# Optimization experiments

Measured on AMD Instinct MI355X. Metric: run time of the kernel, lower is better.

## Reference

```python
import jax, jax.numpy as jnp
import numpy as np

FORGET_BIAS = 1.0
LAYERS = 2


def setup_inputs() -> dict:
    key = jax.random.key(0)
    ks = jax.random.split(key, 10)
    B, T, H, V = 64, 50, 256, 50000
    G = 4 * H
    s = 1.0 / np.sqrt(H)
    return {
        "input_data": jax.random.randint(ks[0], (B, T), 0, V, dtype=jnp.int64),
        "embedding": jax.random.uniform(ks[1], (V, H), jnp.float32, -1.0, 1.0),
        "Wx": jax.random.normal(ks[2], (LAYERS, H, G), jnp.float32) * s,
        "Uh": jax.random.normal(ks[3], (LAYERS, H, G), jnp.float32) * s,
        "alpha": jax.random.uniform(ks[4], (LAYERS, G), jnp.float32),
        "beta1": jax.random.uniform(ks[5], (LAYERS, G), jnp.float32),
        "beta2": jax.random.uniform(ks[6], (LAYERS, G), jnp.float32),
        "bias": jnp.zeros((LAYERS, G), jnp.float32),
        "softmax_w": jax.random.normal(ks[7], (V, H), jnp.float32) * s,
        "softmax_b": jnp.full((V,), 0.1, jnp.float32),
    }


def _mi_lstm_stack(inputs_tbh, Wx, Uh, alpha, beta1, beta2, bias):
    # inputs_tbh: [T, B, H]; params have leading layer axis [L, ...]
    T, B, H = inputs_tbh.shape
    c0 = jnp.zeros((LAYERS, B, H), inputs_tbh.dtype)
    h0 = jnp.zeros((LAYERS, B, H), inputs_tbh.dtype)

    def step(carry, x_t):
        c, h = carry
        inp = x_t
        new_c, new_h = [], []
        for l in range(LAYERS):
            xh = inp @ Wx[l]          # [B, 4H]
            hh = h[l] @ Uh[l]         # [B, 4H]
            gates = alpha[l] * xh * hh + beta1[l] * xh + beta2[l] * hh + bias[l]
            i, j, f, o = jnp.split(gates, 4, axis=-1)
            c_l = c[l] * jax.nn.sigmoid(f + FORGET_BIAS) + jax.nn.sigmoid(i) * jnp.tanh(j)
            h_l = jnp.tanh(c_l) * jax.nn.sigmoid(o)
            new_c.append(c_l)
            new_h.append(h_l)
            inp = h_l
        return (jnp.stack(new_c), jnp.stack(new_h)), inp

    (_, _), outs = jax.lax.scan(step, (c0, h0), inputs_tbh)
    return outs  # [T, B, H] top-layer hidden states


def reference(input_data, embedding, Wx, Uh, alpha, beta1, beta2, bias, softmax_w, softmax_b):
    # embedding lookup: [B, T, H] -> time-major [T, B, H]
    x = embedding[input_data]
    outs = _mi_lstm_stack(jnp.transpose(x, (1, 0, 2)), Wx, Uh, alpha, beta1, beta2, bias)
    # batch-major flatten like tf.reshape(outputs, [-1, rnn_size]) on [B, T, H]
    H = outs.shape[-1]
    flat = jnp.transpose(outs, (1, 0, 2)).reshape(-1, H)  # [B*T, H]
    logits = flat @ softmax_w.T + softmax_b               # [B*T, V]
    return logits
```

## Files before the change

### kernel.cpp

```cpp
#include <hip/hip_runtime.h>
#include <hip/hip_bf16.h>
#include <math.h>

#define B_ 64
#define T_ 50
#define H_ 256
#define G_ 1024
#define V_ 50000
#define NBLK 32

using f16x8 = __attribute__((ext_vector_type(8))) _Float16;
using f32x4 = __attribute__((ext_vector_type(4))) float;

__device__ __forceinline__ float sigm(float x) { return 1.0f / (1.0f + expf(-x)); }

__global__ __launch_bounds__(64) void embed_k(const int* __restrict__ idx,
                                              const float* __restrict__ emb,
                                              float* __restrict__ x_tm)
{
    const int row = blockIdx.x;
    const int b = row & (B_ - 1);
    const int t = row >> 6;
    const int id = idx[b * T_ + t];
    const float4 v = *reinterpret_cast<const float4*>(emb + (size_t)id * H_ + threadIdx.x * 4);
    *reinterpret_cast<float4*>(x_tm + (size_t)row * H_ + threadIdx.x * 4) = v;
}

__global__ __launch_bounds__(256) void conv_half(const float* __restrict__ in,
                                                 _Float16* __restrict__ out, int n)
{
    const int i = (blockIdx.x * 256 + threadIdx.x) * 8;
    if (i + 8 <= n) {
        const float4 v0 = *reinterpret_cast<const float4*>(in + i);
        const float4 v1 = *reinterpret_cast<const float4*>(in + i + 4);
        f16x8 h;
        h[0] = (_Float16)v0.x; h[1] = (_Float16)v0.y;
        h[2] = (_Float16)v0.z; h[3] = (_Float16)v0.w;
        h[4] = (_Float16)v1.x; h[5] = (_Float16)v1.y;
        h[6] = (_Float16)v1.z; h[7] = (_Float16)v1.w;
        *reinterpret_cast<f16x8*>(out + i) = h;
    }
}

__global__ __launch_bounds__(256) void pack_w_rec(const float* __restrict__ Uh0,
                                                  const float* __restrict__ Wx1,
                                                  const float* __restrict__ Uh1,
                                                  _Float16* __restrict__ wpk)
{
    const int c = blockIdx.x;
    const int m = blockIdx.y;
    const float* __restrict__ src = (m == 0) ? Uh0 : (m == 1) ? Wx1 : Uh1;
    _Float16* __restrict__ dst = wpk + (((size_t)c * 3 + m) << 13);
    for (int i = threadIdx.x; i < 8192; i += 256) {
        const int k = i >> 5;
        const int col = i & 31;
        const int colg = ((col >> 3) << 8) + (c << 3) + (col & 7);
        dst[(col << 8) + k] = (_Float16)src[(size_t)k * G_ + colg];
    }
}

__global__ __launch_bounds__(256) void gemm128_kn(const float* __restrict__ A,
                                                  const float* __restrict__ Bm,
                                                  float* __restrict__ C,
                                                  int M, int N, int K)
{
    __shared__ float As[32][132];
    __shared__ float Bs[32][132];

    const int m0 = blockIdx.x * 128;
    const int n0 = blockIdx.y * 128;
    const int tid = threadIdx.x;
    const int tm = (tid >> 4) << 3;
    const int tn = (tid & 15) << 3;

    float acc[8][8];
#pragma unroll
    for (int i = 0; i < 8; ++i)
#pragma unroll
        for (int j = 0; j < 8; ++j) acc[i][j] = 0.0f;

    for (int k0 = 0; k0 < K; k0 += 32) {
#pragma unroll
        for (int i = 0; i < 4; ++i) {
            const int s = tid + (i << 8);
            const int m = s >> 3;
            const int kk = (s & 7) << 2;
            const float4 v = *reinterpret_cast<const float4*>(
                A + (size_t)(m0 + m) * K + k0 + kk);
            As[kk + 0][m] = v.x; As[kk + 1][m] = v.y;
            As[kk + 2][m] = v.z; As[kk + 3][m] = v.w;
        }
#pragma unroll
        for (int i = 0; i < 4; ++i) {
            const int s = tid + (i << 8);
            const int kk = s >> 5;
            const int nn = (s & 31) << 2;
            const float4 v = *reinterpret_cast<const float4*>(
                Bm + (size_t)(k0 + kk) * N + n0 + nn);
            *reinterpret_cast<float4*>(&Bs[kk][nn]) = v;
        }
        __syncthreads();

#pragma unroll
        for (int k = 0; k < 32; ++k) {
            float a[8], bb[8];
            *reinterpret_cast<float4*>(&a[0]) = *reinterpret_cast<const float4*>(&As[k][tm]);
            *reinterpret_cast<float4*>(&a[4]) = *reinterpret_cast<const float4*>(&As[k][tm + 4]);
            *reinterpret_cast<float4*>(&bb[0]) = *reinterpret_cast<const float4*>(&Bs[k][tn]);
            *reinterpret_cast<float4*>(&bb[4]) = *reinterpret_cast<const float4*>(&Bs[k][tn + 4]);
#pragma unroll
            for (int i = 0; i < 8; ++i)
#pragma unroll
                for (int j = 0; j < 8; ++j)
                    acc[i][j] = fmaf(a[i], bb[j], acc[i][j]);
        }
        __syncthreads();
    }

#pragma unroll
    for (int i = 0; i < 8; ++i) {
        const int m = m0 + tm + i;
#pragma unroll
        for (int j = 0; j < 8; j += 4) {
            const int n = n0 + tn + j;
            float4 v;
            v.x = acc[i][j + 0]; v.y = acc[i][j + 1];
            v.z = acc[i][j + 2]; v.w = acc[i][j + 3];
            *reinterpret_cast<float4*>(C + (size_t)m * N + n) = v;
        }
    }
}

__device__ __forceinline__ void gbar_arrive(int* slot)
{
    __syncthreads();
    if (threadIdx.x == 0) {
        __threadfence();
        __hip_atomic_fetch_add(slot, 1, __ATOMIC_RELAXED, __HIP_MEMORY_SCOPE_AGENT);
    }
}

__device__ __forceinline__ void gbar_wait(int* slot)
{
    if (threadIdx.x == 0) {
        while (__hip_atomic_load(slot, __ATOMIC_RELAXED, __HIP_MEMORY_SCOPE_AGENT) < NBLK)
            __builtin_amdgcn_s_sleep(1);
    }
    __syncthreads();
    __threadfence();
}

__global__ __launch_bounds__(256) void mi_rec(
    const _Float16* __restrict__ wpk,
    const float* __restrict__ xh0,
    _Float16* __restrict__ h0x,
    _Float16* __restrict__ h1x,
    _Float16* __restrict__ outsH,
    int* __restrict__ bars,
    const float* __restrict__ alpha, const float* __restrict__ b1,
    const float* __restrict__ b2, const float* __restrict__ bsv)
{
    __shared__ __align__(16) _Float16 h0l[16384];
    __shared__ __align__(16) _Float16 h1l[16384];
    __shared__ __align__(16) _Float16 wl[24576];
    __shared__ float gA[2112], gB[2112];
    __shared__ float c0l[512], c1l[512];

    const int c = blockIdx.x;
    const int tid = threadIdx.x;
    const int l = tid & 63;
    const int w = tid >> 6;

    for (int i = tid; i < 2048; i += 256) {
        *reinterpret_cast<f16x8*>(&h0l[i << 3]) = f16x8{};
        *reinterpret_cast<f16x8*>(&h1l[i << 3]) = f16x8{};
    }
    for (int i = tid; i < 512; i += 256) { c0l[i] = 0.f; c1l[i] = 0.f; }

    for (int i = tid; i < 3072; i += 256) {
        const int m = i >> 10;
        const int col = (i >> 5) & 31;
        const int ch = i & 31;
        const f16x8 v = *reinterpret_cast<const f16x8*>(
            &wpk[(((size_t)c * 3 + m) * 32 + col) * 256 + (ch << 3)]);
        *reinterpret_cast<f16x8*>(
            &wl[(m * 32 + col) * 256 + ((ch ^ (col & 7)) << 3)]) = v;
    }

    const int u = tid & 7, b0 = tid >> 3;
    const int jl = (c << 3) + u;
    float al0[4], b10[4], b20[4], bs0[4], al1[4], b11[4], b21[4], bs1[4];
#pragma unroll
    for (int g = 0; g < 4; ++g) {
        const int col = (g << 8) + jl;
        al0[g] = alpha[col];        b10[g] = b1[col];
        b20[g] = b2[col];           bs0[g] = bsv[col];
        al1[g] = alpha[G_ + col];   b11[g] = b1[G_ + col];
        b21[g] = b2[G_ + col];      bs1[g] = bsv[G_ + col];
    }
    __syncthreads();

    const int arow = (w << 4) + (l & 15);
    const int cA = l & 15, cB = 16 + (l & 15);
    const int kq = l >> 4;

    auto MM = [&](const _Float16* __restrict__ am, const _Float16* __restrict__ bm,
                  f32x4& A0, f32x4& A1) {
#pragma unroll
        for (int s = 0; s < 8; ++s) {
            const int ck = (s << 2) + kq;
            const f16x8 af = *reinterpret_cast<const f16x8*>(
                &am[(arow << 8) + ((ck ^ (arow & 7)) << 3)]);
            const f16x8 bf0 = *reinterpret_cast<const f16x8*>(
                &bm[(cA << 8) + ((ck ^ (cA & 7)) << 3)]);
            const f16x8 bf1 = *reinterpret_cast<const f16x8*>(
                &bm[(cB << 8) + ((ck ^ (cB & 7)) << 3)]);
            A0 = __builtin_amdgcn_mfma_f32_16x16x32_f16(af, bf0, A0, 0, 0, 0);
            A1 = __builtin_amdgcn_mfma_f32_16x16x32_f16(af, bf1, A1, 0, 0, 0);
        }
    };

    auto STG = [&](float* gl, f32x4 A0, f32x4 A1) {
        const int rb = (w << 4) + (kq << 2);
#pragma unroll
        for (int r = 0; r < 4; ++r) {
            gl[(rb + r) * 33 + cA] = A0[r];
            gl[(rb + r) * 33 + cB] = A1[r];
        }
    };

    auto STAGE_H = [&](const _Float16* __restrict__ src, _Float16* __restrict__ dst) {
#pragma unroll
        for (int it = 0; it < 8; ++it) {
            const int idx = (it << 8) + tid;
            const int row = idx >> 5, ch = idx & 31;
            const f16x8 v = *reinterpret_cast<const f16x8*>(&src[(row << 8) + (ch << 3)]);
            *reinterpret_cast<f16x8*>(&dst[(row << 8) + ((ch ^ (row & 7)) << 3)]) = v;
        }
    };

    for (int s = 0; s <= T_; ++s) {
        const int p = s & 1;
        _Float16* __restrict__ h0w = h0x + (p << 14);
        _Float16* __restrict__ h1w = h1x + (p << 14);

        if (s < T_) {
            f32x4 A0 = {}, A1 = {};
            MM(h0l, wl, A0, A1);
            STG(gA, A0, A1);
            __syncthreads();
#pragma unroll
            for (int bb = 0; bb < 2; ++bb) {
                const int b = b0 + (bb << 5);
                float g4[4];
#pragma unroll
                for (int g = 0; g < 4; ++g) {
                    const float a = gA[b * 33 + (g << 3) + u];
                    const float x = xh0[(((size_t)(s * B_ + b)) << 10) + (g << 8) + jl];
                    g4[g] = al0[g] * x * a + b10[g] * x + b20[g] * a + bs0[g];
                }
                const float cn = c0l[(b << 3) + u] * sigm(g4[2] + 1.f)
                               + sigm(g4[0]) * tanhf(g4[1]);
                c0l[(b << 3) + u] = cn;
                h0w[(b << 8) + jl] = (_Float16)(tanhf(cn) * sigm(g4[3]));
            }
            __syncthreads();
        }

        if (s > 0) {
            f32x4 X0 = {}, X1 = {}, H0 = {}, H1 = {};
            MM(h0l, wl + 1 * 8192, X0, X1);
            MM(h1l, wl + 2 * 8192, H0, H1);
            STG(gA, X0, X1);
            STG(gB, H0, H1);
            __syncthreads();
#pragma unroll
            for (int bb = 0; bb < 2; ++bb) {
                const int b = b0 + (bb << 5);
                float g4[4];
#pragma unroll
                for (int g = 0; g < 4; ++g) {
                    const float xa = gA[b * 33 + (g << 3) + u];
                    const float ha = gB[b * 33 + (g << 3) + u];
                    g4[g] = al1[g] * xa * ha + b11[g] * xa + b21[g] * ha + bs1[g];
                }
                const float cn = c1l[(b << 3) + u] * sigm(g4[2] + 1.f)
                               + sigm(g4[0]) * tanhf(g4[1]);
                c1l[(b << 3) + u] = cn;
                const float hn = tanhf(cn) * sigm(g4[3]);
                h1w[(b << 8) + jl] = (_Float16)hn;
                outsH[(((size_t)b * T_ + (s - 1)) << 8) + jl] = (_Float16)hn;
            }
        }

        if (s < T_) {
            gbar_arrive(&bars[s]);
            gbar_wait(&bars[s]);
            STAGE_H(h0w, h0l);
            if (s > 0) STAGE_H(h1w, h1l);
            __syncthreads();
        }
    }
}

#define PM 128
#define PN 128
#define PK 64

__device__ __forceinline__ void gload_lds16(const void* g, void* l)
{
    __builtin_amdgcn_global_load_lds(
        (const __attribute__((address_space(1))) unsigned int*)g,
        (__attribute__((address_space(3))) unsigned int*)l, 16, 0, 0);
}

__global__ __launch_bounds__(256) void proj_mfma(
    const _Float16* __restrict__ A16,
    const _Float16* __restrict__ B16,
    const float* __restrict__ bias,
    float* __restrict__ C)
{
    __shared__ __align__(16) _Float16 Asub[PM * PK];
    __shared__ __align__(16) _Float16 Bsub[PN * PK];

    const int tid = threadIdx.x;
    const int l = tid & 63;
    const int w = tid >> 6;
    const int wm = w >> 1, wn = w & 1;

    const int n0 = blockIdx.x * PN;
    const int m0 = blockIdx.y * PM;

    f32x4 acc[4][4] = {};

    for (int k0 = 0; k0 < H_; k0 += PK) {
#pragma unroll
        for (int is = 0; is < 4; ++is) {
            const int i = is * 256 + tid;
            const int r = i >> 3;
            const int ch = (i & 7) ^ (r & 7);
            gload_lds16(A16 + (size_t)(m0 + r) * H_ + k0 + ch * 8, &Asub[i * 8]);
            int n = n0 + r; if (n > V_ - 1) n = V_ - 1;
            gload_lds16(B16 + (size_t)n * H_ + k0 + ch * 8, &Bsub[i * 8]);
        }
        __syncthreads();

#pragma unroll
        for (int ks = 0; ks < 2; ++ks) {
            f16x8 af[4], bf[4];
#pragma unroll
            for (int i = 0; i < 4; ++i) {
                const int r = wm * 64 + i * 16 + (l & 15);
                const int ch = (ks * 4 + (l >> 4)) ^ (r & 7);
                af[i] = *reinterpret_cast<const f16x8*>(&Asub[r * PK + ch * 8]);
            }
#pragma unroll
            for (int jf = 0; jf < 4; ++jf) {
                const int r = wn * 64 + jf * 16 + (l & 15);
                const int ch = (ks * 4 + (l >> 4)) ^ (r & 7);
                bf[jf] = *reinterpret_cast<const f16x8*>(&Bsub[r * PK + ch * 8]);
            }
#pragma unroll
            for (int i = 0; i < 4; ++i)
#pragma unroll
                for (int jf = 0; jf < 4; ++jf)
                    acc[i][jf] = __builtin_amdgcn_mfma_f32_16x16x32_f16(
                        af[i], bf[jf], acc[i][jf], 0, 0, 0);
        }
        __syncthreads();
    }

    const int rb = (l >> 4) << 2;
    const int cl = l & 15;
#pragma unroll
    for (int jf = 0; jf < 4; ++jf) {
        const int col = n0 + wn * 64 + jf * 16 + cl;
        if (col < V_) {
            const float bv = bias[col];
#pragma unroll
            for (int i = 0; i < 4; ++i) {
                const int rowb = m0 + wm * 64 + i * 16 + rb;
#pragma unroll
                for (int r = 0; r < 4; ++r)
                    C[(size_t)(rowb + r) * V_ + col] = acc[i][jf][r] + bv;
            }
        }
    }
}

extern "C" void kernel_launch(void* const* d_in, const int* in_sizes, int n_in,
                              void* d_out, int out_size, void* d_ws, size_t ws_size,
                              hipStream_t stream)
{
    const int*   idx   = (const int*)  d_in[0];
    const float* emb   = (const float*)d_in[1];
    const float* Wx    = (const float*)d_in[2];
    const float* Uh    = (const float*)d_in[3];
    const float* alpha = (const float*)d_in[4];
    const float* b1    = (const float*)d_in[5];
    const float* b2    = (const float*)d_in[6];
    const float* bsv   = (const float*)d_in[7];
    const float* sw    = (const float*)d_in[8];
    const float* sb    = (const float*)d_in[9];
    float* out = (float*)d_out;

    char* wsb = (char*)d_ws;
    float*    x_tm  = (float*)   (wsb);
    float*    xh0   = (float*)   (wsb + 3276800);
    _Float16* outsH = (_Float16*)(wsb + 16384000);
    _Float16* w16   = (_Float16*)(wsb + 18022400);
    _Float16* wpk   = (_Float16*)(wsb + 43622400);
    _Float16* h0x   = (_Float16*)(wsb + 45195264);
    _Float16* h1x   = (_Float16*)(wsb + 45260800);
    int*      bars  = (int*)     (wsb + 45326336);

    const float* Wx1 = Wx + (size_t)H_ * G_;
    const float* Uh0 = Uh;
    const float* Uh1 = Uh + (size_t)H_ * G_;

    hipMemsetAsync(bars, 0, 512, stream);

    {
        dim3 grid(NBLK, 3);
        pack_w_rec<<<grid, 256, 0, stream>>>(Uh0, Wx1, Uh1, wpk);
    }

    conv_half<<<(V_ * H_) / 2048, 256, 0, stream>>>(sw, w16, V_ * H_);

    embed_k<<<T_ * B_, 64, 0, stream>>>(idx, emb, x_tm);

    {
        dim3 grid(3200 / 128, G_ / 128);
        gemm128_kn<<<grid, 256, 0, stream>>>(x_tm, Wx, xh0, 3200, G_, H_);
    }

    mi_rec<<<NBLK, 256, 0, stream>>>(wpk, xh0, h0x, h1x, outsH, bars,
                                     alpha, b1, b2, bsv);

    {
        dim3 grid((V_ + PN - 1) / PN, 3200 / PM);
        proj_mfma<<<grid, 256, 0, stream>>>(outsH, w16, sb, out);
    }
}
```

Baseline: 724.1 us.

## Use fp16 MFMA for input GEMM, pad barrier slots, reorder projection grid

```diff
diff --git a/kernel.cpp b/kernel.cpp
--- a/kernel.cpp
+++ b/kernel.cpp
@@ -8,22 +8,27 @@
 #define G_ 1024
 #define V_ 50000
 #define NBLK 32
+#define BSTRIDE 64
 
 using f16x8 = __attribute__((ext_vector_type(8))) _Float16;
+using f16x4 = __attribute__((ext_vector_type(4))) _Float16;
 using f32x4 = __attribute__((ext_vector_type(4))) float;
 
 __device__ __forceinline__ float sigm(float x) { return 1.0f / (1.0f + expf(-x)); }
 
 __global__ __launch_bounds__(64) void embed_k(const int* __restrict__ idx,
                                               const float* __restrict__ emb,
-                                              float* __restrict__ x_tm)
+                                              _Float16* __restrict__ x16)
 {
     const int row = blockIdx.x;
     const int b = row & (B_ - 1);
     const int t = row >> 6;
     const int id = idx[b * T_ + t];
     const float4 v = *reinterpret_cast<const float4*>(emb + (size_t)id * H_ + threadIdx.x * 4);
-    *reinterpret_cast<float4*>(x_tm + (size_t)row * H_ + threadIdx.x * 4) = v;
+    f16x4 h;
+    h[0] = (_Float16)v.x; h[1] = (_Float16)v.y;
+    h[2] = (_Float16)v.z; h[3] = (_Float16)v.w;
+    *reinterpret_cast<f16x4*>(x16 + (size_t)row * H_ + threadIdx.x * 4) = h;
 }
 
 __global__ __launch_bounds__(256) void conv_half(const float* __restrict__ in,
@@ -42,6 +47,27 @@
     }
 }
 
+__global__ __launch_bounds__(256) void pack_wx0(const float* __restrict__ Wx0,
+                                                _Float16* __restrict__ wxT)
+{
+    __shared__ _Float16 ts[64][65];
+    const int k0 = blockIdx.x * 64;
+    const int n0 = blockIdx.y * 64;
+    const int tr = threadIdx.x >> 6;
+    const int tc = threadIdx.x & 63;
+#pragma unroll
+    for (int i = 0; i < 16; ++i) {
+        const int r = i * 4 + tr;
+        ts[r][tc] = (_Float16)Wx0[(size_t)(k0 + r) * G_ + n0 + tc];
+    }
+    __syncthreads();
+#pragma unroll
+    for (int i = 0; i < 16; ++i) {
+        const int c = i * 4 + tr;
+        wxT[(size_t)(n0 + c) * H_ + k0 + tc] = ts[tc][c];
+    }
+}
+
 __global__ __launch_bounds__(256) void pack_w_rec(const float* __restrict__ Uh0,
                                                   const float* __restrict__ Wx1,
                                                   const float* __restrict__ Uh1,
@@ -59,76 +85,11 @@
     }
 }
 
-__global__ __launch_bounds__(256) void gemm128_kn(const float* __restrict__ A,
-                                                  const float* __restrict__ Bm,
-                                                  float* __restrict__ C,
-                                                  int M, int N, int K)
-{
-    __shared__ float As[32][132];
-    __shared__ float Bs[32][132];
-
-    const int m0 = blockIdx.x * 128;
-    const int n0 = blockIdx.y * 128;
-    const int tid = threadIdx.x;
-    const int tm = (tid >> 4) << 3;
-    const int tn = (tid & 15) << 3;
-
-    float acc[8][8];
-#pragma unroll
-    for (int i = 0; i < 8; ++i)
-#pragma unroll
-        for (int j = 0; j < 8; ++j) acc[i][j] = 0.0f;
-
-    for (int k0 = 0; k0 < K; k0 += 32) {
-#pragma unroll
-        for (int i = 0; i < 4; ++i) {
-            const int s = tid + (i << 8);
-            const int m = s >> 3;
-            const int kk = (s & 7) << 2;
-            const float4 v = *reinterpret_cast<const float4*>(
-                A + (size_t)(m0 + m) * K + k0 + kk);
-            As[kk + 0][m] = v.x; As[kk + 1][m] = v.y;
-            As[kk + 2][m] = v.z; As[kk + 3][m] = v.w;
-        }
-#pragma unroll
-        for (int i = 0; i < 4; ++i) {
-            const int s = tid + (i << 8);
-            const int kk = s >> 5;
-            const int nn = (s & 31) << 2;
-            const float4 v = *reinterpret_cast<const float4*>(
-                Bm + (size_t)(k0 + kk) * N + n0 + nn);
-            *reinterpret_cast<float4*>(&Bs[kk][nn]) = v;
-        }
-        __syncthreads();
-
-#pragma unroll
-        for (int k = 0; k < 32; ++k) {
-            float a[8], bb[8];
-            *reinterpret_cast<float4*>(&a[0]) = *reinterpret_cast<const float4*>(&As[k][tm]);
-            *reinterpret_cast<float4*>(&a[4]) = *reinterpret_cast<const float4*>(&As[k][tm + 4]);
-            *reinterpret_cast<float4*>(&bb[0]) = *reinterpret_cast<const float4*>(&Bs[k][tn]);
-            *reinterpret_cast<float4*>(&bb[4]) = *reinterpret_cast<const float4*>(&Bs[k][tn + 4]);
-#pragma unroll
-            for (int i = 0; i < 8; ++i)
-#pragma unroll
-                for (int j = 0; j < 8; ++j)
-                    acc[i][j] = fmaf(a[i], bb[j], acc[i][j]);
-        }
-        __syncthreads();
-    }
-
-#pragma unroll
-    for (int i = 0; i < 8; ++i) {
-        const int m = m0 + tm + i;
-#pragma unroll
-        for (int j = 0; j < 8; j += 4) {
-            const int n = n0 + tn + j;
-            float4 v;
-            v.x = acc[i][j + 0]; v.y = acc[i][j + 1];
-            v.z = acc[i][j + 2]; v.w = acc[i][j + 3];
-            *reinterpret_cast<float4*>(C + (size_t)m * N + n) = v;
-        }
-    }
+__device__ __forceinline__ void gload_lds16(const void* g, void* l)
+{
+    __builtin_amdgcn_global_load_lds(
+        (const __attribute__((address_space(1))) unsigned int*)g,
+        (__attribute__((address_space(3))) unsigned int*)l, 16, 0, 0);
 }
 
 __device__ __forceinline__ void gbar_arrive(int* slot)
@@ -140,7 +101,7 @@
     }
 }
 
-__device__ __forceinline__ void gbar_wait(int* slot)
+__device__ __forceinline__ void gbar_wait_fast(int* slot)
 {
     if (threadIdx.x == 0) {
         while (__hip_atomic_load(slot, __ATOMIC_RELAXED, __HIP_MEMORY_SCOPE_AGENT) < NBLK)
@@ -148,6 +109,79 @@
     }
     __syncthreads();
     __threadfence();
+}
+
+#define PM 128
+#define PN 128
+#define PK 64
+
+__global__ __launch_bounds__(256) void gemm16_mfma(
+    const _Float16* __restrict__ A16,
+    const _Float16* __restrict__ B16,
+    float* __restrict__ C)
+{
+    __shared__ __align__(16) _Float16 Asub[PM * PK];
+    __shared__ __align__(16) _Float16 Bsub[PN * PK];
+
+    const int tid = threadIdx.x;
+    const int l = tid & 63;
+    const int w = tid >> 6;
+    const int wm = w >> 1, wn = w & 1;
+
+    const int n0 = blockIdx.x * PN;
+    const int m0 = blockIdx.y * PM;
+
+    f32x4 acc[4][4] = {};
+
+    for (int k0 = 0; k0 < H_; k0 += PK) {
+#pragma unroll
+        for (int is = 0; is < 4; ++is) {
+            const int i = is * 256 + tid;
+            const int r = i >> 3;
+            const int ch = (i & 7) ^ (r & 7);
+            gload_lds16(A16 + (size_t)(m0 + r) * H_ + k0 + ch * 8, &Asub[i * 8]);
+            gload_lds16(B16 + (size_t)(n0 + r) * H_ + k0 + ch * 8, &Bsub[i * 8]);
+        }
+        __syncthreads();
+
+#pragma unroll
+        for (int ks = 0; ks < 2; ++ks) {
+            f16x8 af[4], bf[4];
+#pragma unroll
+            for (int i = 0; i < 4; ++i) {
+                const int r = wm * 64 + i * 16 + (l & 15);
+                const int ch = (ks * 4 + (l >> 4)) ^ (r & 7);
+                af[i] = *reinterpret_cast<const f16x8*>(&Asub[r * PK + ch * 8]);
+            }
+#pragma unroll
+            for (int jf = 0; jf < 4; ++jf) {
+                const int r = wn * 64 + jf * 16 + (l & 15);
+                const int ch = (ks * 4 + (l >> 4)) ^ (r & 7);
+                bf[jf] = *reinterpret_cast<const f16x8*>(&Bsub[r * PK + ch * 8]);
+            }
+#pragma unroll
+            for (int i = 0; i < 4; ++i)
+#pragma unroll
+                for (int jf = 0; jf < 4; ++jf)
+                    acc[i][jf] = __builtin_amdgcn_mfma_f32_16x16x32_f16(
+                        af[i], bf[jf], acc[i][jf], 0, 0, 0);
+        }
+        __syncthreads();
+    }
+
+    const int rb = (l >> 4) << 2;
+    const int cl = l & 15;
+#pragma unroll
+    for (int jf = 0; jf < 4; ++jf) {
+        const int col = n0 + wn * 64 + jf * 16 + cl;
+#pragma unroll
+        for (int i = 0; i < 4; ++i) {
+            const int rowb = m0 + wm * 64 + i * 16 + rb;
+#pragma unroll
+            for (int r = 0; r < 4; ++r)
+                C[(size_t)(rowb + r) * G_ + col] = acc[i][jf][r];
+        }
+    }
 }
 
 __global__ __launch_bounds__(256) void mi_rec(
@@ -204,8 +238,7 @@
     const int cA = l & 15, cB = 16 + (l & 15);
     const int kq = l >> 4;
 
-    auto MM = [&](const _Float16* __restrict__ am, const _Float16* __restrict__ bm,
-                  f32x4& A0, f32x4& A1) {
+    auto MM = [&](const _Float16* am, const _Float16* bm, f32x4& A0, f32x4& A1) {
 #pragma unroll
         for (int s = 0; s < 8; ++s) {
             const int ck = (s << 2) + kq;
@@ -219,7 +252,6 @@
             A1 = __builtin_amdgcn_mfma_f32_16x16x32_f16(af, bf1, A1, 0, 0, 0);
         }
     };
-
     auto STG = [&](float* gl, f32x4 A0, f32x4 A1) {
         const int rb = (w << 4) + (kq << 2);
 #pragma unroll
@@ -228,8 +260,7 @@
             gl[(rb + r) * 33 + cB] = A1[r];
         }
     };
-
-    auto STAGE_H = [&](const _Float16* __restrict__ src, _Float16* __restrict__ dst) {
+    auto STAGE_H = [&](const _Float16* src, _Float16* dst) {
 #pragma unroll
         for (int it = 0; it < 8; ++it) {
             const int idx = (it << 8) + tid;
@@ -241,8 +272,8 @@
 
     for (int s = 0; s <= T_; ++s) {
         const int p = s & 1;
-        _Float16* __restrict__ h0w = h0x + (p << 14);
-        _Float16* __restrict__ h1w = h1x + (p << 14);
+        _Float16* h0w = h0x + (p << 14);
+        _Float16* h1w = h1x + (p << 14);
 
         if (s < T_) {
             f32x4 A0 = {}, A1 = {};
@@ -294,24 +325,13 @@
         }
 
         if (s < T_) {
-            gbar_arrive(&bars[s]);
-            gbar_wait(&bars[s]);
+            gbar_arrive(bars + s * BSTRIDE);
+            gbar_wait_fast(bars + s * BSTRIDE);
             STAGE_H(h0w, h0l);
             if (s > 0) STAGE_H(h1w, h1l);
             __syncthreads();
         }
     }
-}
-
-#define PM 128
-#define PN 128
-#define PK 64
-
-__device__ __forceinline__ void gload_lds16(const void* g, void* l)
-{
-    __builtin_amdgcn_global_load_lds(
-        (const __attribute__((address_space(1))) unsigned int*)g,
-        (__attribute__((address_space(3))) unsigned int*)l, 16, 0, 0);
 }
 
 __global__ __launch_bounds__(256) void proj_mfma(
@@ -328,8 +348,8 @@
     const int w = tid >> 6;
     const int wm = w >> 1, wn = w & 1;
 
-    const int n0 = blockIdx.x * PN;
-    const int m0 = blockIdx.y * PM;
+    const int m0 = blockIdx.x * PM;
+    const int n0 = blockIdx.y * PN;
 
     f32x4 acc[4][4] = {};
 
@@ -405,40 +425,45 @@
     float* out = (float*)d_out;
 
     char* wsb = (char*)d_ws;
-    float*    x_tm  = (float*)   (wsb);
-    float*    xh0   = (float*)   (wsb + 3276800);
-    _Float16* outsH = (_Float16*)(wsb + 16384000);
-    _Float16* w16   = (_Float16*)(wsb + 18022400);
-    _Float16* wpk   = (_Float16*)(wsb + 43622400);
-    _Float16* h0x   = (_Float16*)(wsb + 45195264);
-    _Float16* h1x   = (_Float16*)(wsb + 45260800);
-    int*      bars  = (int*)     (wsb + 45326336);
-
+    _Float16* x16   = (_Float16*)(wsb);
+    float*    xh0   = (float*)   (wsb + 1638400);
+    _Float16* outsH = (_Float16*)(wsb + 14745600);
+    _Float16* w16   = (_Float16*)(wsb + 16384000);
+    _Float16* wxT   = (_Float16*)(wsb + 41984000);
+    _Float16* wpk   = (_Float16*)(wsb + 42508288);
+    _Float16* h0x   = (_Float16*)(wsb + 44081152);
+    _Float16* h1x   = (_Float16*)(wsb + 44146688);
+    int*      bars  = (int*)     (wsb + 44212224);
+
+    const float* Wx0 = Wx;
     const float* Wx1 = Wx + (size_t)H_ * G_;
     const float* Uh0 = Uh;
     const float* Uh1 = Uh + (size_t)H_ * G_;
 
-    hipMemsetAsync(bars, 0, 512, stream);
+    (void)hipMemsetAsync(bars, 0, 16384, stream);
 
     {
         dim3 grid(NBLK, 3);
         pack_w_rec<<<grid, 256, 0, stream>>>(Uh0, Wx1, Uh1, wpk);
     }
-
+    {
+        dim3 grid(4, 16);
+        pack_wx0<<<grid, 256, 0, stream>>>(Wx0, wxT);
+    }
     conv_half<<<(V_ * H_) / 2048, 256, 0, stream>>>(sw, w16, V_ * H_);
 
-    embed_k<<<T_ * B_, 64, 0, stream>>>(idx, emb, x_tm);
+    embed_k<<<T_ * B_, 64, 0, stream>>>(idx, emb, x16);
 
     {
-        dim3 grid(3200 / 128, G_ / 128);
-        gemm128_kn<<<grid, 256, 0, stream>>>(x_tm, Wx, xh0, 3200, G_, H_);
+        dim3 grid(G_ / PN, 3200 / PM);
+        gemm16_mfma<<<grid, 256, 0, stream>>>(x16, wxT, xh0);
     }
 
     mi_rec<<<NBLK, 256, 0, stream>>>(wpk, xh0, h0x, h1x, outsH, bars,
                                      alpha, b1, b2, bsv);
 
     {
-        dim3 grid((V_ + PN - 1) / PN, 3200 / PM);
+        dim3 grid(3200 / PM, (V_ + PN - 1) / PN);
         proj_mfma<<<grid, 256, 0, stream>>>(outsH, w16, sb, out);
     }
 }
```

Result: slower. 751.2 us (+3.7%).
